# Kernel tuning notes

Measured on AMD Instinct MI355X. Metric: run time of the kernel, lower is better.

The kernel has to match this reference:

```python
import jax, jax.numpy as jnp
import numpy as np

C = 128
HEAD_CHANNEL = 32
NUM_HEAD = C // HEAD_CHANNEL
SCALE = HEAD_CHANNEL ** 0.5
EPS = 1e-5


def _layernorm(x, g, b):
    mu = jnp.mean(x, axis=-1, keepdims=True)
    var = jnp.mean((x - mu) ** 2, axis=-1, keepdims=True)
    return (x - mu) * jax.lax.rsqrt(var + EPS) * g + b


def _proj(x, g, b, w1, b1, w2, b2):
    # LayerNorm -> Linear(C,2C) -> LeakyReLU(0.01) -> Linear(2C,C); dropout=0 (identity)
    h = jax.nn.leaky_relu(_layernorm(x, g, b) @ w1 + b1, negative_slope=0.01)
    return h @ w2 + b2


def _mlp(x, w1, b1, w2, b2):
    h = jax.nn.leaky_relu(x @ w1 + b1, negative_slope=0.01)
    return h @ w2 + b2


def setup_inputs() -> dict:
    key = jax.random.key(0)
    ks = jax.random.split(key, 32)
    s = 1.0 / np.sqrt(C)
    s2 = 1.0 / np.sqrt(2 * C)
    d = {}
    d["q"] = jax.random.normal(ks[0], (2, C, 64, 64), jnp.float32)
    d["k"] = jax.random.normal(ks[1], (2, C, 64, 64), jnp.float32)
    d["v"] = jax.random.normal(ks[2], (2, C, 64, 64), jnp.float32)
    i = 3
    for p in ("q", "k", "v"):
        d[f"ln_{p}_g"] = jnp.ones((C,), jnp.float32)
        d[f"ln_{p}_b"] = jnp.zeros((C,), jnp.float32)
        d[f"w{p}1"] = jax.random.uniform(ks[i], (C, 2 * C), jnp.float32, -s, s); i += 1
        d[f"b{p}1"] = jnp.zeros((2 * C,), jnp.float32)
        d[f"w{p}2"] = jax.random.uniform(ks[i], (2 * C, C), jnp.float32, -s2, s2); i += 1
        d[f"b{p}2"] = jnp.zeros((C,), jnp.float32)
    for m in ("m1", "m2"):
        d[f"{m}_w1"] = jax.random.uniform(ks[i], (C, 2 * C), jnp.float32, -s, s); i += 1
        d[f"{m}_b1"] = jnp.zeros((2 * C,), jnp.float32)
        d[f"{m}_w2"] = jax.random.uniform(ks[i], (2 * C, C), jnp.float32, -s2, s2); i += 1
        d[f"{m}_b2"] = jnp.zeros((C,), jnp.float32)
    return d


def reference(q, k, v,
              ln_q_g, ln_q_b, wq1, bq1, wq2, bq2,
              ln_k_g, ln_k_b, wk1, bk1, wk2, bk2,
              ln_v_g, ln_v_b, wv1, bv1, wv2, bv2,
              m1_w1, m1_b1, m1_w2, m1_b2,
              m2_w1, m2_b1, m2_w2, m2_b2):
    B, Cc, H, W = q.shape
    S = H * W
    # [B,C,H,W] -> [B,S,C] token layout
    qt = q.transpose(0, 2, 3, 1).reshape(B, S, Cc)
    kt = k.transpose(0, 2, 3, 1).reshape(B, S, Cc)
    vt = v.transpose(0, 2, 3, 1).reshape(B, S, Cc)
    qp = _proj(qt, ln_q_g, ln_q_b, wq1, bq1, wq2, bq2)
    kp = _proj(kt, ln_k_g, ln_k_b, wk1, bk1, wk2, bk2)
    vp = _proj(vt, ln_v_g, ln_v_b, wv1, bv1, wv2, bv2)  # v_attn_1
    qh = qp.reshape(B, S, NUM_HEAD, HEAD_CHANNEL)
    kh = kp.reshape(B, S, NUM_HEAD, HEAD_CHANNEL)
    vh = vp.reshape(B, S, NUM_HEAD, HEAD_CHANNEL)
    attn = jax.nn.softmax(jnp.einsum('bqhd,bkhd->bhqk', qh, kh) / SCALE, axis=-1)
    x = jnp.einsum('bhqk,bkhd->bqhd', attn, vh).reshape(B, S, Cc)
    rs1 = vp + _mlp(x, m1_w1, m1_b1, m1_w2, m1_b2)
    rs2 = rs1 + _mlp(rs1, m2_w1, m2_b1, m2_w2, m2_b2)
    # back to [B,C,H,W]
    return rs2.reshape(B, H, W, Cc).transpose(0, 3, 1, 2)
```

## Files before the change

kernel.cpp:

```cpp
#include <hip/hip_runtime.h>
#include <hip/hip_bf16.h>

typedef __bf16 bf16_t;
typedef __bf16 bf16x2 __attribute__((ext_vector_type(2)));
typedef __bf16 bf16x4 __attribute__((ext_vector_type(4)));
typedef __bf16 bf16x8 __attribute__((ext_vector_type(8)));
typedef float f32x4 __attribute__((ext_vector_type(4)));
typedef float f32x16 __attribute__((ext_vector_type(16)));


static constexpr size_t WS_WPK   = 0;
static constexpr size_t WS_PP    = 655360;
static constexpr size_t WS_VT    = WS_PP + 3ull*2097152;
static constexpr size_t WS_OPART = WS_VT + 2097152;
static constexpr size_t WS_XN    = WS_OPART;
static constexpr size_t WS_LPART = WS_OPART + 8388608;
static constexpr size_t WS_RS1   = WS_LPART + 524288;

struct WPtrs { const float* w1[5]; const float* w2[5]; };

__global__ __launch_bounds__(256) void prep_weights(WPtrs wp, bf16_t* __restrict__ dst) {
    __shared__ float ts[64][65];
    int bx = blockIdx.x;
    int p = bx >> 4;
    int t = bx & 15;
    const float* src; int sld, dld, r0, c0; bf16_t* d;
    if (t < 8) {
        src = wp.w1[p]; sld = 256; dld = 128;
        r0 = (t >> 2) * 64; c0 = (t & 3) * 64;
        d = dst + p * 65536;
    } else {
        int tt = t - 8;
        src = wp.w2[p]; sld = 128; dld = 256;
        r0 = (tt >> 1) * 64; c0 = (tt & 1) * 64;
        d = dst + p * 65536 + 32768;
    }
    for (int i = threadIdx.x; i < 4096; i += 256) {
        int r = i >> 6, c = i & 63;
        ts[r][c] = src[(r0 + r) * sld + c0 + c];
    }
    __syncthreads();
    for (int i = threadIdx.x; i < 4096; i += 256) {
        int c = i >> 6, r = i & 63;
        d[(c0 + c) * dld + (r0 + r)] = (bf16_t)ts[r][c];
    }
}

struct LNArgs { const float* src[3]; const float* g[3]; const float* bb[3]; bf16_t* dst[3]; };

__global__ __launch_bounds__(256) void ln_kernel(LNArgs a) {
    __shared__ float xs[64][129];
    __shared__ float mu_s[64], rs_s[64];
    int z = blockIdx.y;
    int t0 = blockIdx.x * 64;
    int b = t0 >> 12;
    int s0 = t0 & 4095;
    const float* src = a.src[z];
    for (int idx = threadIdx.x; idx < 128 * 64; idx += 256) {
        int c = idx >> 6, tx = idx & 63;
        xs[tx][c] = src[(b * 128 + c) * 4096 + s0 + tx];
    }
    __syncthreads();
    {
        int t = threadIdx.x >> 2, jj = threadIdx.x & 3;
        float sum = 0.f, sq = 0.f;
#pragma unroll
        for (int ci = 0; ci < 32; ++ci) {
            float v = xs[t][ci * 4 + jj];
            sum += v; sq += v * v;
        }
        sum += __shfl_xor(sum, 1); sq += __shfl_xor(sq, 1);
        sum += __shfl_xor(sum, 2); sq += __shfl_xor(sq, 2);
        if (jj == 0) {
            float mu = sum * (1.0f / 128.0f);
            float var = sq * (1.0f / 128.0f) - mu * mu;
            mu_s[t] = mu;
            rs_s[t] = rsqrtf(var + 1e-5f);
        }
    }
    __syncthreads();
    const float* g = a.g[z];
    const float* bb = a.bb[z];
    bf16_t* dst = a.dst[z];
    for (int idx = threadIdx.x; idx < 64 * 128; idx += 256) {
        int t = idx >> 7, c = idx & 127;
        float v = (xs[t][c] - mu_s[t]) * rs_s[t] * g[c] + bb[c];
        dst[(t0 + t) * 128 + c] = (bf16_t)v;
    }
}

struct MlpArgs {
    const bf16_t* A[3];
    const bf16_t* W1T[3];
    const float* B1[3];
    const bf16_t* W2T[3];
    const float* B2[3];
    const bf16_t* RESP[3];
    bf16_t* OUT[3];
    bf16_t* VTOUT[3];
    float* FOUT;
};

template <bool RESF, bool FOUTF>
__global__ __launch_bounds__(256) void mlp_kernel(MlpArgs a) {
    __shared__ bf16_t hl[16][264];
    int z = blockIdx.y;
    int w = threadIdx.x >> 6;
    int lane = threadIdx.x & 63;
    int quad = lane >> 4;
    int l15 = lane & 15;
    int m0 = blockIdx.x * 16;

    const bf16_t* arow = a.A[z] + (size_t)(m0 + l15) * 128 + quad * 8;
    bf16x8 af[4];
#pragma unroll
    for (int kt = 0; kt < 4; ++kt) af[kt] = *(const bf16x8*)(arow + kt * 32);

#pragma unroll
    for (int sub = 0; sub < 4; ++sub) {
        int n = w * 64 + sub * 16 + l15;
        const bf16_t* wrow = a.W1T[z] + (size_t)n * 128 + quad * 8;
        f32x4 acc = {0.f, 0.f, 0.f, 0.f};
#pragma unroll
        for (int kt = 0; kt < 4; ++kt) {
            bf16x8 bfrag = *(const bf16x8*)(wrow + kt * 32);
            acc = __builtin_amdgcn_mfma_f32_16x16x32_bf16(af[kt], bfrag, acc, 0, 0, 0);
        }
        float bn = a.B1[z][n];
#pragma unroll
        for (int r = 0; r < 4; ++r) {
            float v = acc[r] + bn;
            v = v > 0.f ? v : 0.01f * v;
            hl[quad * 4 + r][n] = (bf16_t)v;
        }
    }
    __syncthreads();

    bf16x8 hf[8];
#pragma unroll
    for (int kt = 0; kt < 8; ++kt)
        hf[kt] = *(const bf16x8*)(&hl[l15][kt * 32 + quad * 8]);

#pragma unroll
    for (int sub = 0; sub < 2; ++sub) {
        int n = w * 32 + sub * 16 + l15;
        const bf16_t* wrow = a.W2T[z] + (size_t)n * 256 + quad * 8;
        f32x4 acc = {0.f, 0.f, 0.f, 0.f};
#pragma unroll
        for (int kt = 0; kt < 8; ++kt) {
            bf16x8 bfrag = *(const bf16x8*)(wrow + kt * 32);
            acc = __builtin_amdgcn_mfma_f32_16x16x32_bf16(hf[kt], bfrag, acc, 0, 0, 0);
        }
        float bn = a.B2[z][n];
        float vals[4];
#pragma unroll
        for (int r = 0; r < 4; ++r) {
            int m = m0 + quad * 4 + r;
            float v = acc[r] + bn;
            if (RESF) v += (float)a.RESP[z][(size_t)m * 128 + n];
            vals[r] = v;
        }
        if constexpr (FOUTF) {
            int b = m0 >> 12, s0 = m0 & 4095;
            f32x4 ov = {vals[0], vals[1], vals[2], vals[3]};
            *(f32x4*)(a.FOUT + ((size_t)(b * 128 + n)) * 4096 + s0 + quad * 4) = ov;
        } else {
#pragma unroll
            for (int r = 0; r < 4; ++r)
                a.OUT[z][(size_t)(m0 + quad * 4 + r) * 128 + n] = (bf16_t)vals[r];
            if (a.VTOUT[z] != nullptr) {
                int b = m0 >> 12, s0 = m0 & 4095;
                int bh = b * 4 + (n >> 5), d = n & 31;
                bf16x4 tv = {(bf16_t)vals[0], (bf16_t)vals[1], (bf16_t)vals[2], (bf16_t)vals[3]};
                *(bf16x4*)(a.VTOUT[z] + ((size_t)(bh * 32 + d)) * 4096 + s0 + quad * 4) = tv;
            }
        }
    }
}

__global__ __launch_bounds__(256) void attn_kernel(const bf16_t* __restrict__ qp,
                                                   const bf16_t* __restrict__ kp,
                                                   const bf16_t* __restrict__ vt,
                                                   bf16_t* __restrict__ opart,
                                                   float* __restrict__ lpart) {
    int lid = blockIdx.x;
    int bh = lid & 7;
    int r = lid >> 3;
    int split = r & 3;
    int qb = r >> 2;
    int w = threadIdx.x >> 6;
    int lane = threadIdx.x & 63;
    int l31 = lane & 31;
    int h5 = lane >> 5;
    int b = bh >> 2, h = bh & 3;
    int q0 = qb * 128 + w * 32;

    constexpr float kScale = 0.17677669529663687f * 1.4426950408889634f;

    const bf16_t* qrow = qp + ((size_t)(b * 4096 + q0 + l31)) * 128 + h * 32 + h5 * 8;
    bf16x8 qr0 = *(const bf16x8*)(qrow);
    bf16x8 qr1 = *(const bf16x8*)(qrow + 16);
    bf16x8 qf0, qf1;
#pragma unroll
    for (int j = 0; j < 8; ++j) {
        qf0[j] = (bf16_t)((float)qr0[j] * kScale);
        qf1[j] = (bf16_t)((float)qr1[j] * kScale);
    }

    int key_m = (l31 & ~12) | ((l31 & 4) << 1) | ((l31 & 8) >> 1);
    const bf16_t* kbase = kp + ((size_t)(b * 4096) + key_m) * 128 + h * 32 + h5 * 8;
    const bf16_t* vbase = vt + ((size_t)(bh * 32) + l31) * 4096 + h5 * 8;

    f32x16 acc = {0.f,0.f,0.f,0.f,0.f,0.f,0.f,0.f,0.f,0.f,0.f,0.f,0.f,0.f,0.f,0.f};
    f32x16 lacc = acc;
    f32x16 zero16 = acc;

    int kt0 = split * 32;
    const bf16_t* kpt = kbase + (size_t)kt0 * 4096;
    const bf16_t* vpt = vbase + kt0 * 32;
    bf16x8 kf0 = *(const bf16x8*)(kpt);
    bf16x8 kf1 = *(const bf16x8*)(kpt + 16);
    bf16x8 vf0 = *(const bf16x8*)(vpt);
    bf16x8 vf1 = *(const bf16x8*)(vpt + 16);

    for (int it = 0; it < 32; ++it) {
        const bf16_t* nkpt = kpt + (it < 31 ? 4096 : 0);
        const bf16_t* nvpt = vpt + (it < 31 ? 32 : 0);
        bf16x8 nk0 = *(const bf16x8*)(nkpt);
        bf16x8 nk1 = *(const bf16x8*)(nkpt + 16);
        bf16x8 nv0 = *(const bf16x8*)(nvpt);
        bf16x8 nv1 = *(const bf16x8*)(nvpt + 16);

        f32x16 sc = __builtin_amdgcn_mfma_f32_32x32x16_bf16(kf0, qf0, zero16, 0, 0, 0);
        sc = __builtin_amdgcn_mfma_f32_32x32x16_bf16(kf1, qf1, sc, 0, 0, 0);

        float p[16];
#pragma unroll
        for (int i = 0; i < 16; ++i) {
            p[i] = __builtin_amdgcn_exp2f(sc[i]);
            lacc[i] += p[i];
        }

        bf16x8 pf0, pf1;
#pragma unroll
        for (int j = 0; j < 8; ++j) { pf0[j] = (bf16_t)p[j]; pf1[j] = (bf16_t)p[8 + j]; }

        acc = __builtin_amdgcn_mfma_f32_32x32x16_bf16(vf0, pf0, acc, 0, 0, 0);
        acc = __builtin_amdgcn_mfma_f32_32x32x16_bf16(vf1, pf1, acc, 0, 0, 0);

        kf0 = nk0; kf1 = nk1; vf0 = nv0; vf1 = nv1;
        kpt = nkpt; vpt = nvpt;
    }

    float l_lane = (((lacc[0] + lacc[1]) + (lacc[2] + lacc[3])) +
                    ((lacc[4] + lacc[5]) + (lacc[6] + lacc[7]))) +
                   (((lacc[8] + lacc[9]) + (lacc[10] + lacc[11])) +
                    ((lacc[12] + lacc[13]) + (lacc[14] + lacc[15])));
    float l_tot = l_lane + __shfl_xor(l_lane, 32);

    size_t obase = ((size_t)(bh * 4 + split) * 4096 + q0 + l31) * 32;
#pragma unroll
    for (int g = 0; g < 4; ++g) {
        bf16x4 ov = {(bf16_t)acc[4 * g], (bf16_t)acc[4 * g + 1], (bf16_t)acc[4 * g + 2], (bf16_t)acc[4 * g + 3]};
        *(bf16x4*)(opart + obase + 8 * g + 4 * h5) = ov;
    }
    lpart[(bh * 4 + split) * 4096 + q0 + l31] = l_tot;
}

__global__ __launch_bounds__(256) void mlp1_kernel(const bf16_t* __restrict__ opart,
                                                   const float* __restrict__ lpart,
                                                   const bf16_t* __restrict__ w1t,
                                                   const float* __restrict__ b1,
                                                   const bf16_t* __restrict__ w2t,
                                                   const float* __restrict__ b2,
                                                   const bf16_t* __restrict__ resp,
                                                   bf16_t* __restrict__ outp) {
    __shared__ bf16_t al[16][136];
    __shared__ bf16_t hl[16][264];
    int w = threadIdx.x >> 6;
    int lane = threadIdx.x & 63;
    int quad = lane >> 4;
    int l15 = lane & 15;
    int m0 = blockIdx.x * 16;

    {
        int t = threadIdx.x >> 4;
        int cg = threadIdx.x & 15;
        int m = m0 + t;
        int b = m >> 12, qq = m & 4095;
        int h = cg >> 2, d0 = (cg & 3) * 8;
        int bh = b * 4 + h;
        float accv[8] = {0.f, 0.f, 0.f, 0.f, 0.f, 0.f, 0.f, 0.f};
        float l = 0.f;
#pragma unroll
        for (int s = 0; s < 4; ++s) {
            const bf16_t* op = opart + ((size_t)((bh * 4 + s) * 4096) + qq) * 32 + d0;
            bf16x8 o8 = *(const bf16x8*)op;
#pragma unroll
            for (int j = 0; j < 8; ++j) accv[j] += (float)o8[j];
            l += lpart[(bh * 4 + s) * 4096 + qq];
        }
        float invl = 1.0f / l;
        bf16x8 a8;
#pragma unroll
        for (int j = 0; j < 8; ++j) a8[j] = (bf16_t)(accv[j] * invl);
        *(bf16x8*)(&al[t][cg * 8]) = a8;
    }
    __syncthreads();

    bf16x8 af[4];
#pragma unroll
    for (int kt = 0; kt < 4; ++kt) af[kt] = *(const bf16x8*)(&al[l15][kt * 32 + quad * 8]);

#pragma unroll
    for (int sub = 0; sub < 4; ++sub) {
        int n = w * 64 + sub * 16 + l15;
        const bf16_t* wrow = w1t + (size_t)n * 128 + quad * 8;
        f32x4 acc = {0.f, 0.f, 0.f, 0.f};
#pragma unroll
        for (int kt = 0; kt < 4; ++kt) {
            bf16x8 bfrag = *(const bf16x8*)(wrow + kt * 32);
            acc = __builtin_amdgcn_mfma_f32_16x16x32_bf16(af[kt], bfrag, acc, 0, 0, 0);
        }
        float bn = b1[n];
#pragma unroll
        for (int r = 0; r < 4; ++r) {
            float v = acc[r] + bn;
            v = v > 0.f ? v : 0.01f * v;
            hl[quad * 4 + r][n] = (bf16_t)v;
        }
    }
    __syncthreads();

    bf16x8 hf[8];
#pragma unroll
    for (int kt = 0; kt < 8; ++kt)
        hf[kt] = *(const bf16x8*)(&hl[l15][kt * 32 + quad * 8]);

#pragma unroll
    for (int sub = 0; sub < 2; ++sub) {
        int n = w * 32 + sub * 16 + l15;
        const bf16_t* wrow = w2t + (size_t)n * 256 + quad * 8;
        f32x4 acc = {0.f, 0.f, 0.f, 0.f};
#pragma unroll
        for (int kt = 0; kt < 8; ++kt) {
            bf16x8 bfrag = *(const bf16x8*)(wrow + kt * 32);
            acc = __builtin_amdgcn_mfma_f32_16x16x32_bf16(hf[kt], bfrag, acc, 0, 0, 0);
        }
        float bn = b2[n];
#pragma unroll
        for (int r = 0; r < 4; ++r) {
            int m = m0 + quad * 4 + r;
            float v = acc[r] + bn + (float)resp[(size_t)m * 128 + n];
            outp[(size_t)m * 128 + n] = (bf16_t)v;
        }
    }
}

extern "C" void kernel_launch(void* const* d_in, const int* in_sizes, int n_in,
                              void* d_out, int out_size, void* d_ws, size_t ws_size,
                              hipStream_t stream) {
    const float* q = (const float*)d_in[0];
    const float* k = (const float*)d_in[1];
    const float* v = (const float*)d_in[2];
    const float* ln_g[3] = {(const float*)d_in[3], (const float*)d_in[9], (const float*)d_in[15]};
    const float* ln_b[3] = {(const float*)d_in[4], (const float*)d_in[10], (const float*)d_in[16]};
    const float* w1[5] = {(const float*)d_in[5], (const float*)d_in[11], (const float*)d_in[17],
                          (const float*)d_in[21], (const float*)d_in[25]};
    const float* b1[5] = {(const float*)d_in[6], (const float*)d_in[12], (const float*)d_in[18],
                          (const float*)d_in[22], (const float*)d_in[26]};
    const float* w2[5] = {(const float*)d_in[7], (const float*)d_in[13], (const float*)d_in[19],
                          (const float*)d_in[23], (const float*)d_in[27]};
    const float* b2[5] = {(const float*)d_in[8], (const float*)d_in[14], (const float*)d_in[20],
                          (const float*)d_in[24], (const float*)d_in[28]};
    float* out = (float*)d_out;

    char* ws = (char*)d_ws;
    bf16_t* wpk = (bf16_t*)(ws + WS_WPK);
    bf16_t* pp  = (bf16_t*)(ws + WS_PP);
    bf16_t* vtb = (bf16_t*)(ws + WS_VT);
    bf16_t* xn  = (bf16_t*)(ws + WS_XN);
    bf16_t* opart = (bf16_t*)(ws + WS_OPART);
    float* lpart = (float*)(ws + WS_LPART);
    bf16_t* rs1 = (bf16_t*)(ws + WS_RS1);

    WPtrs wp;
    for (int p = 0; p < 5; ++p) { wp.w1[p] = w1[p]; wp.w2[p] = w2[p]; }
    prep_weights<<<80, 256, 0, stream>>>(wp, wpk);

    LNArgs la;
    la.src[0] = q; la.src[1] = k; la.src[2] = v;
    for (int i = 0; i < 3; ++i) { la.g[i] = ln_g[i]; la.bb[i] = ln_b[i]; la.dst[i] = xn + (size_t)i * 1048576; }
    ln_kernel<<<dim3(128, 3), 256, 0, stream>>>(la);

    MlpArgs pa;
    for (int p = 0; p < 3; ++p) {
        pa.A[p] = xn + (size_t)p * 1048576;
        pa.W1T[p] = wpk + (size_t)p * 65536; pa.B1[p] = b1[p];
        pa.W2T[p] = wpk + (size_t)p * 65536 + 32768; pa.B2[p] = b2[p];
        pa.RESP[p] = nullptr;
        pa.OUT[p] = pp + (size_t)p * 1048576;
        pa.VTOUT[p] = (p == 2) ? vtb : nullptr;
    }
    pa.FOUT = nullptr;
    mlp_kernel<false, false><<<dim3(512, 3), 256, 0, stream>>>(pa);

    attn_kernel<<<1024, 256, 0, stream>>>(pp, pp + 1048576, vtb, opart, lpart);

    mlp1_kernel<<<512, 256, 0, stream>>>(opart, lpart,
                                         wpk + 3ull * 65536, b1[3],
                                         wpk + 3ull * 65536 + 32768, b2[3],
                                         pp + 2ull * 1048576, rs1);

    MlpArgs m2;
    m2.A[0] = rs1; m2.W1T[0] = wpk + 4ull * 65536; m2.B1[0] = b1[4];
    m2.W2T[0] = wpk + 4ull * 65536 + 32768; m2.B2[0] = b2[4];
    m2.RESP[0] = rs1; m2.OUT[0] = nullptr; m2.VTOUT[0] = nullptr; m2.FOUT = out;
    m2.A[1] = m2.A[2] = nullptr; m2.W1T[1] = m2.W1T[2] = nullptr;
    m2.B1[1] = m2.B1[2] = nullptr; m2.W2T[1] = m2.W2T[2] = nullptr;
    m2.B2[1] = m2.B2[2] = nullptr; m2.RESP[1] = m2.RESP[2] = nullptr;
    m2.OUT[1] = m2.OUT[2] = nullptr; m2.VTOUT[1] = m2.VTOUT[2] = nullptr;
    mlp_kernel<true, true><<<dim3(512, 1), 256, 0, stream>>>(m2);
}
```

Measured before the change: 240.8 us.

## Double query rows per attention wave, sum softmax on MFMA, merge prep kernels

Each attention wave now handles 64 query rows instead of 32, so every loaded K/V fragment feeds two score and PV MFMA pairs and the grid halves. The per-row probability sums move from VALU adds to MFMAs against constant one/zero selector matrices, which frees VALU work but adds four extra MFMAs per iteration. The weight transpose and LayerNorm kernels are merged into one launch to drop one kernel launch. Register pressure rises from the two accumulators, and occupancy is capped with launch_bounds(256,2).

```diff
diff --git a/kernel.cpp b/kernel.cpp
--- a/kernel.cpp
+++ b/kernel.cpp
@@ -17,75 +17,77 @@
 static constexpr size_t WS_LPART = WS_OPART + 8388608;
 static constexpr size_t WS_RS1   = WS_LPART + 524288;
 
-struct WPtrs { const float* w1[5]; const float* w2[5]; };
-
-__global__ __launch_bounds__(256) void prep_weights(WPtrs wp, bf16_t* __restrict__ dst) {
-    __shared__ float ts[64][65];
-    int bx = blockIdx.x;
-    int p = bx >> 4;
-    int t = bx & 15;
-    const float* src; int sld, dld, r0, c0; bf16_t* d;
-    if (t < 8) {
-        src = wp.w1[p]; sld = 256; dld = 128;
-        r0 = (t >> 2) * 64; c0 = (t & 3) * 64;
-        d = dst + p * 65536;
-    } else {
-        int tt = t - 8;
-        src = wp.w2[p]; sld = 128; dld = 256;
-        r0 = (tt >> 1) * 64; c0 = (tt & 1) * 64;
-        d = dst + p * 65536 + 32768;
-    }
-    for (int i = threadIdx.x; i < 4096; i += 256) {
-        int r = i >> 6, c = i & 63;
-        ts[r][c] = src[(r0 + r) * sld + c0 + c];
-    }
-    __syncthreads();
-    for (int i = threadIdx.x; i < 4096; i += 256) {
-        int c = i >> 6, r = i & 63;
-        d[(c0 + c) * dld + (r0 + r)] = (bf16_t)ts[r][c];
-    }
-}
-
-struct LNArgs { const float* src[3]; const float* g[3]; const float* bb[3]; bf16_t* dst[3]; };
-
-__global__ __launch_bounds__(256) void ln_kernel(LNArgs a) {
+struct PrepArgs {
+    const float* src[3]; const float* g[3]; const float* bb[3]; bf16_t* dst[3];
+    const float* w1[5]; const float* w2[5]; bf16_t* wdst;
+};
+
+__global__ __launch_bounds__(256) void prep_kernel(PrepArgs a) {
     __shared__ float xs[64][129];
     __shared__ float mu_s[64], rs_s[64];
-    int z = blockIdx.y;
-    int t0 = blockIdx.x * 64;
-    int b = t0 >> 12;
-    int s0 = t0 & 4095;
-    const float* src = a.src[z];
-    for (int idx = threadIdx.x; idx < 128 * 64; idx += 256) {
-        int c = idx >> 6, tx = idx & 63;
-        xs[tx][c] = src[(b * 128 + c) * 4096 + s0 + tx];
-    }
-    __syncthreads();
-    {
-        int t = threadIdx.x >> 2, jj = threadIdx.x & 3;
-        float sum = 0.f, sq = 0.f;
-#pragma unroll
-        for (int ci = 0; ci < 32; ++ci) {
-            float v = xs[t][ci * 4 + jj];
-            sum += v; sq += v * v;
-        }
-        sum += __shfl_xor(sum, 1); sq += __shfl_xor(sq, 1);
-        sum += __shfl_xor(sum, 2); sq += __shfl_xor(sq, 2);
-        if (jj == 0) {
-            float mu = sum * (1.0f / 128.0f);
-            float var = sq * (1.0f / 128.0f) - mu * mu;
-            mu_s[t] = mu;
-            rs_s[t] = rsqrtf(var + 1e-5f);
-        }
-    }
-    __syncthreads();
-    const float* g = a.g[z];
-    const float* bb = a.bb[z];
-    bf16_t* dst = a.dst[z];
-    for (int idx = threadIdx.x; idx < 64 * 128; idx += 256) {
-        int t = idx >> 7, c = idx & 127;
-        float v = (xs[t][c] - mu_s[t]) * rs_s[t] * g[c] + bb[c];
-        dst[(t0 + t) * 128 + c] = (bf16_t)v;
+    int bx = blockIdx.x;
+    if (bx < 384) {
+        int z = bx >> 7;
+        int t0 = (bx & 127) * 64;
+        int b = t0 >> 12;
+        int s0 = t0 & 4095;
+        const float* src = a.src[z];
+        for (int idx = threadIdx.x; idx < 128 * 64; idx += 256) {
+            int c = idx >> 6, tx = idx & 63;
+            xs[tx][c] = src[(b * 128 + c) * 4096 + s0 + tx];
+        }
+        __syncthreads();
+        {
+            int t = threadIdx.x >> 2, jj = threadIdx.x & 3;
+            float sum = 0.f, sq = 0.f;
+#pragma unroll
+            for (int ci = 0; ci < 32; ++ci) {
+                float v = xs[t][ci * 4 + jj];
+                sum += v; sq += v * v;
+            }
+            sum += __shfl_xor(sum, 1); sq += __shfl_xor(sq, 1);
+            sum += __shfl_xor(sum, 2); sq += __shfl_xor(sq, 2);
+            if (jj == 0) {
+                float mu = sum * (1.0f / 128.0f);
+                float var = sq * (1.0f / 128.0f) - mu * mu;
+                mu_s[t] = mu;
+                rs_s[t] = rsqrtf(var + 1e-5f);
+            }
+        }
+        __syncthreads();
+        const float* g = a.g[z];
+        const float* bb = a.bb[z];
+        bf16_t* dst = a.dst[z];
+        for (int idx = threadIdx.x; idx < 64 * 128; idx += 256) {
+            int t = idx >> 7, c = idx & 127;
+            float v = (xs[t][c] - mu_s[t]) * rs_s[t] * g[c] + bb[c];
+            dst[(t0 + t) * 128 + c] = (bf16_t)v;
+        }
+    } else {
+        float (*ts)[65] = (float(*)[65])xs;
+        int wx = bx - 384;
+        int p = wx >> 4;
+        int t = wx & 15;
+        const float* src; int sld, dld, r0, c0; bf16_t* d;
+        if (t < 8) {
+            src = a.w1[p]; sld = 256; dld = 128;
+            r0 = (t >> 2) * 64; c0 = (t & 3) * 64;
+            d = a.wdst + p * 65536;
+        } else {
+            int tt = t - 8;
+            src = a.w2[p]; sld = 128; dld = 256;
+            r0 = (tt >> 1) * 64; c0 = (tt & 1) * 64;
+            d = a.wdst + p * 65536 + 32768;
+        }
+        for (int i = threadIdx.x; i < 4096; i += 256) {
+            int r = i >> 6, c = i & 63;
+            ts[r][c] = src[(r0 + r) * sld + c0 + c];
+        }
+        __syncthreads();
+        for (int i = threadIdx.x; i < 4096; i += 256) {
+            int c = i >> 6, r = i & 63;
+            d[(c0 + c) * dld + (r0 + r)] = (bf16_t)ts[r][c];
+        }
     }
 }
 
@@ -178,11 +180,11 @@
     }
 }
 
-__global__ __launch_bounds__(256) void attn_kernel(const bf16_t* __restrict__ qp,
-                                                   const bf16_t* __restrict__ kp,
-                                                   const bf16_t* __restrict__ vt,
-                                                   bf16_t* __restrict__ opart,
-                                                   float* __restrict__ lpart) {
+__global__ __launch_bounds__(256, 2) void attn_kernel(const bf16_t* __restrict__ qp,
+                                                      const bf16_t* __restrict__ kp,
+                                                      const bf16_t* __restrict__ vt,
+                                                      bf16_t* __restrict__ opart,
+                                                      float* __restrict__ lpart) {
     int lid = blockIdx.x;
     int bh = lid & 7;
     int r = lid >> 3;
@@ -193,27 +195,37 @@
     int l31 = lane & 31;
     int h5 = lane >> 5;
     int b = bh >> 2, h = bh & 3;
-    int q0 = qb * 128 + w * 32;
+    int q0 = qb * 256 + w * 64;
 
     constexpr float kScale = 0.17677669529663687f * 1.4426950408889634f;
 
-    const bf16_t* qrow = qp + ((size_t)(b * 4096 + q0 + l31)) * 128 + h * 32 + h5 * 8;
-    bf16x8 qr0 = *(const bf16x8*)(qrow);
-    bf16x8 qr1 = *(const bf16x8*)(qrow + 16);
-    bf16x8 qf0, qf1;
-#pragma unroll
-    for (int j = 0; j < 8; ++j) {
-        qf0[j] = (bf16_t)((float)qr0[j] * kScale);
-        qf1[j] = (bf16_t)((float)qr1[j] * kScale);
+    bf16x8 qf[2][2];
+#pragma unroll
+    for (int s = 0; s < 2; ++s) {
+        const bf16_t* qrow = qp + ((size_t)(b * 4096 + q0 + s * 32 + l31)) * 128 + h * 32 + h5 * 8;
+        bf16x8 q0r = *(const bf16x8*)(qrow);
+        bf16x8 q1r = *(const bf16x8*)(qrow + 16);
+#pragma unroll
+        for (int j = 0; j < 8; ++j) {
+            qf[s][0][j] = (bf16_t)((float)q0r[j] * kScale);
+            qf[s][1][j] = (bf16_t)((float)q1r[j] * kScale);
+        }
+    }
+
+    bf16x8 a_up, a_lo;
+    {
+        bf16_t one = (bf16_t)1.0f, zer = (bf16_t)0.0f;
+#pragma unroll
+        for (int j = 0; j < 8; ++j) { a_up[j] = (l31 < 16) ? one : zer; a_lo[j] = (l31 < 16) ? zer : one; }
     }
 
     int key_m = (l31 & ~12) | ((l31 & 4) << 1) | ((l31 & 8) >> 1);
     const bf16_t* kbase = kp + ((size_t)(b * 4096) + key_m) * 128 + h * 32 + h5 * 8;
     const bf16_t* vbase = vt + ((size_t)(bh * 32) + l31) * 4096 + h5 * 8;
 
-    f32x16 acc = {0.f,0.f,0.f,0.f,0.f,0.f,0.f,0.f,0.f,0.f,0.f,0.f,0.f,0.f,0.f,0.f};
-    f32x16 lacc = acc;
-    f32x16 zero16 = acc;
+    f32x16 acca = {0.f,0.f,0.f,0.f,0.f,0.f,0.f,0.f,0.f,0.f,0.f,0.f,0.f,0.f,0.f,0.f};
+    f32x16 accb = acca, lacc = acca;
+    f32x16 zero16 = acca;
 
     int kt0 = split * 32;
     const bf16_t* kpt = kbase + (size_t)kt0 * 4096;
@@ -231,40 +243,47 @@
         bf16x8 nv0 = *(const bf16x8*)(nvpt);
         bf16x8 nv1 = *(const bf16x8*)(nvpt + 16);
 
-        f32x16 sc = __builtin_amdgcn_mfma_f32_32x32x16_bf16(kf0, qf0, zero16, 0, 0, 0);
-        sc = __builtin_amdgcn_mfma_f32_32x32x16_bf16(kf1, qf1, sc, 0, 0, 0);
-
-        float p[16];
-#pragma unroll
-        for (int i = 0; i < 16; ++i) {
-            p[i] = __builtin_amdgcn_exp2f(sc[i]);
-            lacc[i] += p[i];
-        }
-
-        bf16x8 pf0, pf1;
-#pragma unroll
-        for (int j = 0; j < 8; ++j) { pf0[j] = (bf16_t)p[j]; pf1[j] = (bf16_t)p[8 + j]; }
-
-        acc = __builtin_amdgcn_mfma_f32_32x32x16_bf16(vf0, pf0, acc, 0, 0, 0);
-        acc = __builtin_amdgcn_mfma_f32_32x32x16_bf16(vf1, pf1, acc, 0, 0, 0);
+        f32x16 sca = __builtin_amdgcn_mfma_f32_32x32x16_bf16(kf0, qf[0][0], zero16, 0, 0, 0);
+        sca = __builtin_amdgcn_mfma_f32_32x32x16_bf16(kf1, qf[0][1], sca, 0, 0, 0);
+        f32x16 scb = __builtin_amdgcn_mfma_f32_32x32x16_bf16(kf0, qf[1][0], zero16, 0, 0, 0);
+        scb = __builtin_amdgcn_mfma_f32_32x32x16_bf16(kf1, qf[1][1], scb, 0, 0, 0);
+
+        bf16x8 pfa0, pfa1, pfb0, pfb1;
+#pragma unroll
+        for (int j = 0; j < 8; ++j) {
+            pfa0[j] = (bf16_t)__builtin_amdgcn_exp2f(sca[j]);
+            pfa1[j] = (bf16_t)__builtin_amdgcn_exp2f(sca[8 + j]);
+            pfb0[j] = (bf16_t)__builtin_amdgcn_exp2f(scb[j]);
+            pfb1[j] = (bf16_t)__builtin_amdgcn_exp2f(scb[8 + j]);
+        }
+
+        lacc = __builtin_amdgcn_mfma_f32_32x32x16_bf16(a_up, pfa0, lacc, 0, 0, 0);
+        lacc = __builtin_amdgcn_mfma_f32_32x32x16_bf16(a_up, pfa1, lacc, 0, 0, 0);
+        lacc = __builtin_amdgcn_mfma_f32_32x32x16_bf16(a_lo, pfb0, lacc, 0, 0, 0);
+        lacc = __builtin_amdgcn_mfma_f32_32x32x16_bf16(a_lo, pfb1, lacc, 0, 0, 0);
+
+        acca = __builtin_amdgcn_mfma_f32_32x32x16_bf16(vf0, pfa0, acca, 0, 0, 0);
+        acca = __builtin_amdgcn_mfma_f32_32x32x16_bf16(vf1, pfa1, acca, 0, 0, 0);
+        accb = __builtin_amdgcn_mfma_f32_32x32x16_bf16(vf0, pfb0, accb, 0, 0, 0);
+        accb = __builtin_amdgcn_mfma_f32_32x32x16_bf16(vf1, pfb1, accb, 0, 0, 0);
 
         kf0 = nk0; kf1 = nk1; vf0 = nv0; vf1 = nv1;
         kpt = nkpt; vpt = nvpt;
     }
 
-    float l_lane = (((lacc[0] + lacc[1]) + (lacc[2] + lacc[3])) +
-                    ((lacc[4] + lacc[5]) + (lacc[6] + lacc[7]))) +
-                   (((lacc[8] + lacc[9]) + (lacc[10] + lacc[11])) +
-                    ((lacc[12] + lacc[13]) + (lacc[14] + lacc[15])));
-    float l_tot = l_lane + __shfl_xor(l_lane, 32);
-
-    size_t obase = ((size_t)(bh * 4 + split) * 4096 + q0 + l31) * 32;
+    size_t obase0 = ((size_t)(bh * 4 + split) * 4096 + q0 + l31) * 32;
 #pragma unroll
     for (int g = 0; g < 4; ++g) {
-        bf16x4 ov = {(bf16_t)acc[4 * g], (bf16_t)acc[4 * g + 1], (bf16_t)acc[4 * g + 2], (bf16_t)acc[4 * g + 3]};
-        *(bf16x4*)(opart + obase + 8 * g + 4 * h5) = ov;
-    }
-    lpart[(bh * 4 + split) * 4096 + q0 + l31] = l_tot;
+        bf16x4 ov = {(bf16_t)acca[4*g], (bf16_t)acca[4*g+1], (bf16_t)acca[4*g+2], (bf16_t)acca[4*g+3]};
+        *(bf16x4*)(opart + obase0 + 8 * g + 4 * h5) = ov;
+    }
+    size_t obase1 = obase0 + 32ull * 32;
+#pragma unroll
+    for (int g = 0; g < 4; ++g) {
+        bf16x4 ov = {(bf16_t)accb[4*g], (bf16_t)accb[4*g+1], (bf16_t)accb[4*g+2], (bf16_t)accb[4*g+3]};
+        *(bf16x4*)(opart + obase1 + 8 * g + 4 * h5) = ov;
+    }
+    lpart[(bh * 4 + split) * 4096 + q0 + h5 * 32 + l31] = h5 ? lacc[8] : lacc[0];
 }
 
 __global__ __launch_bounds__(256) void mlp1_kernel(const bf16_t* __restrict__ opart,
@@ -384,14 +403,12 @@
     float* lpart = (float*)(ws + WS_LPART);
     bf16_t* rs1 = (bf16_t*)(ws + WS_RS1);
 
-    WPtrs wp;
-    for (int p = 0; p < 5; ++p) { wp.w1[p] = w1[p]; wp.w2[p] = w2[p]; }
-    prep_weights<<<80, 256, 0, stream>>>(wp, wpk);
-
-    LNArgs la;
-    la.src[0] = q; la.src[1] = k; la.src[2] = v;
-    for (int i = 0; i < 3; ++i) { la.g[i] = ln_g[i]; la.bb[i] = ln_b[i]; la.dst[i] = xn + (size_t)i * 1048576; }
-    ln_kernel<<<dim3(128, 3), 256, 0, stream>>>(la);
+    PrepArgs pra;
+    pra.src[0] = q; pra.src[1] = k; pra.src[2] = v;
+    for (int i = 0; i < 3; ++i) { pra.g[i] = ln_g[i]; pra.bb[i] = ln_b[i]; pra.dst[i] = xn + (size_t)i * 1048576; }
+    for (int p = 0; p < 5; ++p) { pra.w1[p] = w1[p]; pra.w2[p] = w2[p]; }
+    pra.wdst = wpk;
+    prep_kernel<<<464, 256, 0, stream>>>(pra);
 
     MlpArgs pa;
     for (int p = 0; p < 3; ++p) {
@@ -405,7 +422,7 @@
     pa.FOUT = nullptr;
     mlp_kernel<false, false><<<dim3(512, 3), 256, 0, stream>>>(pa);
 
-    attn_kernel<<<1024, 256, 0, stream>>>(pp, pp + 1048576, vtb, opart, lpart);
+    attn_kernel<<<512, 256, 0, stream>>>(pp, pp + 1048576, vtb, opart, lpart);
 
     mlp1_kernel<<<512, 256, 0, stream>>>(opart, lpart,
                                          wpk + 3ull * 65536, b1[3],
```

Measured after the change: 208.0 us. 13.6% less time.
